# Performance work log

Hardware: AMD Instinct MI355X
Metric: run time of the kernel (lower is better)

Reference implementation:

```python
import jax, jax.numpy as jnp
import numpy as np

B, T, E, H = 8, 4096, 1024, 128

def setup_inputs() -> dict:
    key = jax.random.key(0)
    kx, kq, kk, kv = jax.random.split(key, 4)
    x = jax.random.normal(kx, (B, T, E), dtype=jnp.float32)
    # bias-free Linear weights stored as (in, out) for x @ W
    scale = 1.0 / np.sqrt(E)
    Wq = jax.random.normal(kq, (E, H), dtype=jnp.float32) * scale
    Wk = jax.random.normal(kk, (E, H), dtype=jnp.float32) * scale
    Wv = jax.random.normal(kv, (E, H), dtype=jnp.float32) * scale
    return {"x": x, "Wq": Wq, "Wk": Wk, "Wv": Wv}

def reference(x, Wq, Wk, Wv):
    # x: (B,T,E) -> out: (B,T,H). Causal single-head attention, dropout p=0 (no-op).
    q = x @ Wq  # (B,T,H)
    k = x @ Wk
    v = x @ Wv
    head_norm = jnp.sqrt(jnp.float32(q.shape[-1]))
    att = jnp.einsum('bth,bsh->bts', q, k) / head_norm  # (B,T,T)
    causal = jnp.tril(jnp.ones((x.shape[1], x.shape[1]), dtype=bool))
    att = jnp.where(causal, att, -jnp.inf)
    att = jax.nn.softmax(att, axis=-1)
    return jnp.einsum('bts,bsh->bth', att, v)
```

## Files before the change

kernel.cpp:

```cpp
#include <hip/hip_runtime.h>
#include <hip/hip_bf16.h>
#include <stdint.h>

#define Bn 8
#define Tn 4096
#define En 1024
#define Hn 128
#define SCALE 0.08838834764831845f

typedef __attribute__((ext_vector_type(8))) short bf16x8;
typedef __attribute__((ext_vector_type(4))) float f32x4;

__device__ __forceinline__ float bf2f(unsigned short v) {
    return __uint_as_float(((unsigned int)v) << 16);
}
__device__ __forceinline__ unsigned int pkbf(float a, float b) {
    __hip_bfloat162 h = __float22bfloat162_rn(make_float2(a, b));
    union { __hip_bfloat162 h2; unsigned int u; } cv;
    cv.h2 = h;
    return cv.u;
}

__device__ __forceinline__ void gll16(const unsigned short* g, unsigned short* l) {
    __builtin_amdgcn_global_load_lds(
        (const __attribute__((address_space(1))) void*)g,
        (__attribute__((address_space(3))) void*)l, 16, 0, 0);
}

__global__ __launch_bounds__(256)
void xcvt(const float* __restrict__ x, unsigned short* __restrict__ xb) {
    const size_t i = ((size_t)blockIdx.x * 256 + threadIdx.x) * 16;
    const float4* src = (const float4*)(x + i);
    float4 a = src[0], b = src[1], c = src[2], d = src[3];
    uint4 o0, o1;
    o0.x = pkbf(a.x, a.y); o0.y = pkbf(a.z, a.w);
    o0.z = pkbf(b.x, b.y); o0.w = pkbf(b.z, b.w);
    o1.x = pkbf(c.x, c.y); o1.y = pkbf(c.z, c.w);
    o1.z = pkbf(d.x, d.y); o1.w = pkbf(d.z, d.w);
    *(uint4*)(xb + i) = o0;
    *(uint4*)(xb + i + 8) = o1;
}

__global__ __launch_bounds__(256)
void wcvt(const float* __restrict__ Wq, const float* __restrict__ Wk,
          const float* __restrict__ Wv, unsigned short* __restrict__ wt3) {
    const int which = blockIdx.x;
    const int k0 = blockIdx.y * 128;
    const float* W = (which == 0) ? Wq : (which == 1) ? Wk : Wv;
    unsigned short* wt = wt3 + (size_t)which * 131072;

    __shared__ unsigned short wl[128 * 132];
    const int t = threadIdx.x;
#pragma unroll
    for (int i = 0; i < 16; ++i) {
        const int idx = t + i * 256;
        const int k = idx >> 5, c4 = idx & 31;
        float4 v = *(const float4*)&W[(size_t)(k0 + k) * Hn + c4 * 4];
        uint2 p;
        p.x = pkbf(v.x, v.y);
        p.y = pkbf(v.z, v.w);
        *(uint2*)&wl[k * 132 + c4 * 4] = p;
    }
    __syncthreads();
#pragma unroll
    for (int j = 0; j < 32; ++j) {
        const int idx = t + j * 256;
        const int n = idx >> 6, kp = idx & 63;
        unsigned int u = (unsigned int)wl[(2 * kp) * 132 + n] |
                         ((unsigned int)wl[(2 * kp + 1) * 132 + n] << 16);
        *(unsigned int*)&wt[(size_t)n * 1024 + k0 + 2 * kp] = u;
    }
}

#define QSWZ(r, c) (((r) << 7) + ((c) ^ (((r) & 7) << 4)))

__global__ __launch_bounds__(256)
void qkv2(const unsigned short* __restrict__ xb,
          const unsigned short* __restrict__ wt3,
          unsigned short* __restrict__ Qo,
          unsigned short* __restrict__ Ko,
          unsigned short* __restrict__ Vo) {
    const int mt = blockIdx.x;
    const int which = blockIdx.y;
    const unsigned short* wt = wt3 + (size_t)which * 131072;
    unsigned short* out = (which == 0) ? Qo : (which == 1) ? Ko : Vo;
    const float scale = (which == 0) ? SCALE : 1.0f;

    __shared__ alignas(16) unsigned short Xs[2][128 * 64];
    __shared__ alignas(16) unsigned short Ws[2][128 * 64];

    const int t = threadIdx.x;
    const int w = t >> 6;
    const int lane = t & 63;
    const int quad = lane >> 4;
    const int l16 = lane & 15;
    const int r8 = lane >> 3;
    const int cb = lane & 7;

    const unsigned short* xtile = xb + (size_t)(mt * 128) * En;

    f32x4 acc[2][8];
#pragma unroll
    for (int mi = 0; mi < 2; ++mi)
#pragma unroll
        for (int nst = 0; nst < 8; ++nst) acc[mi][nst] = (f32x4){0.f, 0.f, 0.f, 0.f};

    auto stage = [&](int buf, int kt) {
#pragma unroll
        for (int i = 0; i < 4; ++i) {
            const int row = i * 32 + w * 8 + r8;
            gll16(xtile + (size_t)row * En + kt * 64 + ((cb ^ (row & 7)) * 8),
                  &Xs[buf][(i * 32 + w * 8) * 64]);
        }
#pragma unroll
        for (int i = 0; i < 4; ++i) {
            const int row = i * 32 + w * 8 + r8;
            gll16(wt + (size_t)row * 1024 + kt * 64 + ((cb ^ (row & 7)) * 8),
                  &Ws[buf][(i * 32 + w * 8) * 64]);
        }
    };

    stage(0, 0);
    __syncthreads();

    for (int kt = 0; kt < 16; ++kt) {
        const int buf = kt & 1;
        if (kt < 15) stage(buf ^ 1, kt + 1);
        const char* xs = (const char*)Xs[buf];
        const char* ws = (const char*)Ws[buf];
#pragma unroll
        for (int ks = 0; ks < 2; ++ks) {
            bf16x8 af[2];
#pragma unroll
            for (int mi = 0; mi < 2; ++mi)
                af[mi] = *(const bf16x8*)(xs + QSWZ(w * 32 + mi * 16 + l16, ks * 64 + quad * 16));
#pragma unroll
            for (int nst = 0; nst < 8; ++nst) {
                bf16x8 bfr = *(const bf16x8*)(ws + QSWZ(nst * 16 + l16, ks * 64 + quad * 16));
                acc[0][nst] = __builtin_amdgcn_mfma_f32_16x16x32_bf16(bfr, af[0], acc[0][nst], 0, 0, 0);
                acc[1][nst] = __builtin_amdgcn_mfma_f32_16x16x32_bf16(bfr, af[1], acc[1][nst], 0, 0, 0);
            }
        }
        if (kt < 15) __syncthreads();
    }

#pragma unroll
    for (int mi = 0; mi < 2; ++mi) {
        const size_t rowbase = (size_t)(mt * 128 + w * 32 + mi * 16 + l16) * Hn;
#pragma unroll
        for (int nst = 0; nst < 8; ++nst) {
            f32x4 v = acc[mi][nst];
            uint2 pk;
            pk.x = pkbf(v[0] * scale, v[1] * scale);
            pk.y = pkbf(v[2] * scale, v[3] * scale);
            *(uint2*)(out + rowbase + nst * 16 + quad * 4) = pk;
        }
    }
}

__global__ __launch_bounds__(256)
void qkv_mfma(const float* __restrict__ x,
              const float* __restrict__ Wq,
              const float* __restrict__ Wk,
              const float* __restrict__ Wv,
              unsigned short* __restrict__ Qo,
              unsigned short* __restrict__ Ko,
              unsigned short* __restrict__ Vo) {
    const int mt = blockIdx.x;
    const int which = blockIdx.y;
    const float* W = (which == 0) ? Wq : (which == 1) ? Wk : Wv;
    unsigned short* out = (which == 0) ? Qo : (which == 1) ? Ko : Vo;
    const float scale = (which == 0) ? SCALE : 1.0f;

    __shared__ alignas(16) unsigned short Xs[128 * 72];
    __shared__ alignas(16) unsigned short Wt[128 * 72];

    const int t = threadIdx.x;
    const int w = t >> 6;
    const int lane = t & 63;
    const int quad = lane >> 4;
    const int l16 = lane & 15;

    const int xrow = t >> 1;
    const int xkc = (t & 1) * 32;
    const int ws0 = (t & 31) * 2;
    const int wd0 = (t >> 5) * 16;

    const float* xsrc0 = x + (size_t)(mt * 128 + xrow) * En + xkc;

    f32x4 acc[2][8];
#pragma unroll
    for (int mi = 0; mi < 2; ++mi)
#pragma unroll
        for (int nst = 0; nst < 8; ++nst) acc[mi][nst] = (f32x4){0.f, 0.f, 0.f, 0.f};

    float4 xpre[8], wpre[8];
    {
        const float* src = xsrc0;
#pragma unroll
        for (int i = 0; i < 8; ++i) xpre[i] = *(const float4*)(src + i * 4);
        const float* w0 = W + (size_t)ws0 * Hn + wd0;
        const float* w1 = w0 + Hn;
#pragma unroll
        for (int i = 0; i < 4; ++i) wpre[i] = *(const float4*)(w0 + i * 4);
#pragma unroll
        for (int i = 0; i < 4; ++i) wpre[4 + i] = *(const float4*)(w1 + i * 4);
    }

    for (int kt = 0; kt < 16; ++kt) {
        __syncthreads();
        {
            unsigned int u[16];
#pragma unroll
            for (int i = 0; i < 8; ++i) {
                u[2 * i]     = pkbf(xpre[i].x, xpre[i].y);
                u[2 * i + 1] = pkbf(xpre[i].z, xpre[i].w);
            }
#pragma unroll
            for (int i = 0; i < 4; ++i)
                *(uint4*)&Xs[xrow * 72 + xkc + i * 8] = ((const uint4*)u)[i];

            const float* ax = (const float*)&wpre[0];
            const float* bx = (const float*)&wpre[4];
#pragma unroll
            for (int dd = 0; dd < 16; ++dd)
                *(unsigned int*)&Wt[(wd0 + dd) * 72 + ws0] = pkbf(ax[dd], bx[dd]);
        }
        if (kt < 15) {
            const float* src = xsrc0 + (kt + 1) * 64;
#pragma unroll
            for (int i = 0; i < 8; ++i) xpre[i] = *(const float4*)(src + i * 4);
            const float* w0 = W + (size_t)((kt + 1) * 64 + ws0) * Hn + wd0;
            const float* w1 = w0 + Hn;
#pragma unroll
            for (int i = 0; i < 4; ++i) wpre[i] = *(const float4*)(w0 + i * 4);
#pragma unroll
            for (int i = 0; i < 4; ++i) wpre[4 + i] = *(const float4*)(w1 + i * 4);
        }
        __syncthreads();

#pragma unroll
        for (int ks = 0; ks < 2; ++ks) {
            bf16x8 af[2];
#pragma unroll
            for (int mi = 0; mi < 2; ++mi)
                af[mi] = *(const bf16x8*)&Xs[(w * 32 + mi * 16 + l16) * 72 + ks * 32 + quad * 8];
#pragma unroll
            for (int nst = 0; nst < 8; ++nst) {
                bf16x8 bfr = *(const bf16x8*)&Wt[(nst * 16 + l16) * 72 + ks * 32 + quad * 8];
                acc[0][nst] = __builtin_amdgcn_mfma_f32_16x16x32_bf16(bfr, af[0], acc[0][nst], 0, 0, 0);
                acc[1][nst] = __builtin_amdgcn_mfma_f32_16x16x32_bf16(bfr, af[1], acc[1][nst], 0, 0, 0);
            }
        }
    }

#pragma unroll
    for (int mi = 0; mi < 2; ++mi) {
        const size_t rowbase = (size_t)(mt * 128 + w * 32 + mi * 16 + l16) * Hn;
#pragma unroll
        for (int nst = 0; nst < 8; ++nst) {
            f32x4 v = acc[mi][nst];
            uint2 pk;
            pk.x = pkbf(v[0] * scale, v[1] * scale);
            pk.y = pkbf(v[2] * scale, v[3] * scale);
            *(uint2*)(out + rowbase + nst * 16 + quad * 4) = pk;
        }
    }
}

#define KSWZ(r, c) (((r) << 8) + ((c) ^ (((r) & 7) << 4)))
#define VSWZ(r, c) (((r) << 7) + ((c) ^ (((r) & 7) << 4)))

__global__ __launch_bounds__(512, 4)
void flash_mfma(const unsigned short* __restrict__ Qb,
                const unsigned short* __restrict__ Kb,
                const unsigned short* __restrict__ Vb,
                float* __restrict__ out) {
    const int b = blockIdx.x;
    const int bx = blockIdx.y;
    const int qt = (bx < 32) ? (63 - bx) : (bx - 32);
    const int t = threadIdx.x;
    const int w = t >> 6;
    const int g = w >> 2;
    const int rg = w & 3;
    const int lane = t & 63;
    const int quad = lane >> 4;
    const int l16 = lane & 15;
    const int t256 = t & 255;

    extern __shared__ unsigned short pool[];
    char* const poolb = (char*)pool;
    char* const Kg = poolb + g * 16384;
    char* const Vg = poolb + 32768 + g * 16384;
    char* const Pw = poolb + 65536 + w * 2048;
    float* const Os = (float*)poolb;
    float* const Ex = (float*)(poolb + 40960);
    float* const Em = (float*)(poolb + 73728);
    float* const El = Em + 64;

    const size_t gbase = (size_t)b * ((size_t)Tn * Hn);
    const unsigned short* kbase = Kb + gbase;
    const unsigned short* vbase = Vb + gbase;

    const int l_hi = lane >> 4;
    const int cpr = (lane & 15) * 16;
    const int vs0 = (t256 & 31) * 2;
    const int vd0 = (t256 >> 5) * 16;

    uint4 vra, vrb, vrc, vrd;
    if (g <= qt) {
        const unsigned short* vsrc = vbase + (size_t)(g * 64) * Hn;
        vra = *(const uint4*)&vsrc[vs0 * 128 + vd0];
        vrb = *(const uint4*)&vsrc[vs0 * 128 + vd0 + 8];
        vrc = *(const uint4*)&vsrc[(vs0 + 1) * 128 + vd0];
        vrd = *(const uint4*)&vsrc[(vs0 + 1) * 128 + vd0 + 8];
    }

    {
        const unsigned short* qsrc = Qb + gbase + (size_t)(qt * 64) * Hn;
#pragma unroll
        for (int i = 0; i < 2; ++i) {
            const int row = w * 8 + i * 4 + l_hi;
            const int scol = cpr ^ ((row & 7) << 4);
            gll16(qsrc + row * 128 + (scol >> 1),
                  (unsigned short*)(poolb + w * 2048 + i * 1024));
        }
    }
    __syncthreads();

    bf16x8 qf[4];
#pragma unroll
    for (int ks = 0; ks < 4; ++ks)
        qf[ks] = *(const bf16x8*)(poolb + KSWZ(rg * 16 + l16, ks * 64 + quad * 16));

    f32x4 acc_o[8];
#pragma unroll
    for (int i = 0; i < 8; ++i) acc_o[i] = (f32x4){0.f, 0.f, 0.f, 0.f};
    float m_run = -1e30f, l_run = 0.f;

    const int n = (qt >> 1) + 1;
    for (int it = 0; it < n; ++it) {
        const int kt = 2 * it + g;
        const bool active = (kt <= qt);
        __syncthreads();
        if (active) {
            const unsigned short* ktile = kbase + (size_t)(kt * 64) * Hn;
#pragma unroll
            for (int i = 0; i < 4; ++i) {
                const int row = rg * 16 + i * 4 + l_hi;
                const int scol = cpr ^ ((row & 7) << 4);
                gll16(ktile + row * 128 + (scol >> 1),
                      (unsigned short*)(Kg + rg * 4096 + i * 1024));
            }
            const unsigned short* pa = (const unsigned short*)&vra;
            const unsigned short* pb = (const unsigned short*)&vrb;
            const unsigned short* pc = (const unsigned short*)&vrc;
            const unsigned short* pd = (const unsigned short*)&vrd;
#pragma unroll
            for (int dd = 0; dd < 8; ++dd)
                *(unsigned int*)(Vg + VSWZ(vd0 + dd, vs0 * 2)) =
                    (unsigned int)pa[dd] | ((unsigned int)pc[dd] << 16);
#pragma unroll
            for (int dd = 0; dd < 8; ++dd)
                *(unsigned int*)(Vg + VSWZ(vd0 + 8 + dd, vs0 * 2)) =
                    (unsigned int)pb[dd] | ((unsigned int)pd[dd] << 16);
        }
        __syncthreads();
        if (kt + 2 <= qt) {
            const unsigned short* vsrc = vbase + (size_t)((kt + 2) * 64) * Hn;
            vra = *(const uint4*)&vsrc[vs0 * 128 + vd0];
            vrb = *(const uint4*)&vsrc[vs0 * 128 + vd0 + 8];
            vrc = *(const uint4*)&vsrc[(vs0 + 1) * 128 + vd0];
            vrd = *(const uint4*)&vsrc[(vs0 + 1) * 128 + vd0 + 8];
        }
        if (!active) continue;

        const bool diag = (kt == qt);
        f32x4 sa[4];
#pragma unroll
        for (int st = 0; st < 4; ++st) {
            if (diag && st > rg) {
                sa[st] = (f32x4){-1e30f, -1e30f, -1e30f, -1e30f};
            } else {
                f32x4 c = (f32x4){0.f, 0.f, 0.f, 0.f};
#pragma unroll
                for (int ks = 0; ks < 4; ++ks) {
                    bf16x8 kf = *(const bf16x8*)(Kg + KSWZ(st * 16 + l16, ks * 64 + quad * 16));
                    c = __builtin_amdgcn_mfma_f32_16x16x32_bf16(kf, qf[ks], c, 0, 0, 0);
                }
                if (diag && st == rg) {
#pragma unroll
                    for (int r = 0; r < 4; ++r)
                        if (quad * 4 + r > l16) c[r] = -1e30f;
                }
                sa[st] = c;
            }
        }

        float mloc = -1e30f;
#pragma unroll
        for (int st = 0; st < 4; ++st)
#pragma unroll
            for (int r = 0; r < 4; ++r) mloc = fmaxf(mloc, sa[st][r]);
        mloc = fmaxf(mloc, __shfl_xor(mloc, 16));
        mloc = fmaxf(mloc, __shfl_xor(mloc, 32));
        const float m_new = fmaxf(m_run, mloc);
        const float alpha = __expf(m_run - m_new);
        float lsum = 0.f;
#pragma unroll
        for (int st = 0; st < 4; ++st)
#pragma unroll
            for (int r = 0; r < 4; ++r) {
                const float e = __expf(sa[st][r] - m_new);
                sa[st][r] = e;
                lsum += e;
            }
        lsum += __shfl_xor(lsum, 16);
        lsum += __shfl_xor(lsum, 32);
        l_run = l_run * alpha + lsum;
        m_run = m_new;
#pragma unroll
        for (int i = 0; i < 8; ++i) acc_o[i] *= alpha;

#pragma unroll
        for (int st = 0; st < 4; ++st) {
            uint2 pk;
            pk.x = pkbf(sa[st][0], sa[st][1]);
            pk.y = pkbf(sa[st][2], sa[st][3]);
            *(uint2*)(Pw + VSWZ(l16, st * 32 + quad * 8)) = pk;
        }
        bf16x8 pf0 = *(const bf16x8*)(Pw + VSWZ(l16, quad * 16));
        bf16x8 pf1 = *(const bf16x8*)(Pw + VSWZ(l16, 64 + quad * 16));

#pragma unroll
        for (int dt = 0; dt < 8; ++dt) {
            bf16x8 vf0 = *(const bf16x8*)(Vg + VSWZ(dt * 16 + l16, quad * 16));
            acc_o[dt] = __builtin_amdgcn_mfma_f32_16x16x32_bf16(vf0, pf0, acc_o[dt], 0, 0, 0);
            bf16x8 vf1 = *(const bf16x8*)(Vg + VSWZ(dt * 16 + l16, 64 + quad * 16));
            acc_o[dt] = __builtin_amdgcn_mfma_f32_16x16x32_bf16(vf1, pf1, acc_o[dt], 0, 0, 0);
        }
    }

    __syncthreads();
    if (g == 1) {
        float* dst = Ex + (rg * 16 + l16) * 128;
#pragma unroll
        for (int dt = 0; dt < 8; ++dt)
            *(f32x4*)&dst[dt * 16 + quad * 4] = acc_o[dt];
        if (quad == 0) {
            Em[rg * 16 + l16] = m_run;
            El[rg * 16 + l16] = l_run;
        }
    }
    __syncthreads();
    if (g == 0) {
        const float* src = Ex + (rg * 16 + l16) * 128;
        const float m2 = Em[rg * 16 + l16];
        const float l2 = El[rg * 16 + l16];
        const float ms = fmaxf(m_run, m2);
        const float a1 = __expf(m_run - ms);
        const float a2 = __expf(m2 - ms);
        const float linv = 1.f / (l_run * a1 + l2 * a2);
#pragma unroll
        for (int dt = 0; dt < 8; ++dt) {
            f32x4 o2 = *(const f32x4*)&src[dt * 16 + quad * 4];
            f32x4 v = (acc_o[dt] * a1 + o2 * a2) * linv;
            *(f32x4*)&Os[(rg * 16 + l16) * 132 + dt * 16 + quad * 4] = v;
        }
    }
    __syncthreads();
    float* dst = out + gbase + (size_t)(qt * 64) * Hn;
#pragma unroll
    for (int i = 0; i < 4; ++i) {
        const int idx = (t + i * 512) * 4;
        const int row = idx >> 7, col = idx & 127;
        *(float4*)&dst[row * 128 + col] = *(const float4*)&Os[row * 132 + col];
    }
}

extern "C" void kernel_launch(void* const* d_in, const int* in_sizes, int n_in,
                              void* d_out, int out_size, void* d_ws, size_t ws_size,
                              hipStream_t stream) {
    const float* x  = (const float*)d_in[0];
    const float* Wq = (const float*)d_in[1];
    const float* Wk = (const float*)d_in[2];
    const float* Wv = (const float*)d_in[3];
    float* o = (float*)d_out;

    const size_t qkvb = (size_t)Bn * Tn * Hn;
    unsigned short* Qb = (unsigned short*)d_ws;
    unsigned short* Kb = Qb + qkvb;
    unsigned short* Vb = Kb + qkvb;
    unsigned short* xbf = Vb + qkvb;
    unsigned short* wt3 = xbf + (size_t)Bn * Tn * En;

    const size_t ws_need = (3 * qkvb + (size_t)Bn * Tn * En + 3 * (size_t)Hn * En)
                           * sizeof(unsigned short);

    static bool attr_done = false;
    if (!attr_done) {
        hipFuncSetAttribute((const void*)flash_mfma,
                            hipFuncAttributeMaxDynamicSharedMemorySize, 81920);
        attr_done = true;
    }

    if (ws_size >= ws_need) {
        xcvt<<<8192, 256, 0, stream>>>(x, xbf);
        wcvt<<<dim3(3, 8), 256, 0, stream>>>(Wq, Wk, Wv, wt3);
        qkv2<<<dim3(256, 3), 256, 0, stream>>>(xbf, wt3, Qb, Kb, Vb);
    } else {
        qkv_mfma<<<dim3(256, 3), 256, 0, stream>>>(x, Wq, Wk, Wv, Qb, Kb, Vb);
    }
    flash_mfma<<<dim3(8, 64), 512, 81920, stream>>>(Qb, Kb, Vb, o);
}
```

Measured before the change: 356.5 us.

## Halve flash block to 4 waves, each computing two 16-row query strips

The attention kernel now launches 256 threads (4 waves) per block instead of 512. Each wave handles 32 query rows as two 16-row sub-tiles and reuses every K fragment loaded from LDS across both sub-tiles, and every V fragment across both P operands. This cuts LDS reads per MFMA and barrier participants, but doubles the accumulator and Q-fragment registers per wave, which lowers occupancy. Each thread also stages twice as much of the K/V tile, and the number of blocks is unchanged.

```diff
diff --git a/kernel.cpp b/kernel.cpp
--- a/kernel.cpp
+++ b/kernel.cpp
@@ -271,7 +271,7 @@
 #define KSWZ(r, c) (((r) << 8) + ((c) ^ (((r) & 7) << 4)))
 #define VSWZ(r, c) (((r) << 7) + ((c) ^ (((r) & 7) << 4)))
 
-__global__ __launch_bounds__(512, 4)
+__global__ __launch_bounds__(256, 2)
 void flash_mfma(const unsigned short* __restrict__ Qb,
                 const unsigned short* __restrict__ Kb,
                 const unsigned short* __restrict__ Vb,
@@ -281,18 +281,18 @@
     const int qt = (bx < 32) ? (63 - bx) : (bx - 32);
     const int t = threadIdx.x;
     const int w = t >> 6;
-    const int g = w >> 2;
-    const int rg = w & 3;
+    const int g = w >> 1;
+    const int rg = w & 1;
     const int lane = t & 63;
     const int quad = lane >> 4;
     const int l16 = lane & 15;
-    const int t256 = t & 255;
+    const int t128 = t & 127;
 
     extern __shared__ unsigned short pool[];
     char* const poolb = (char*)pool;
     char* const Kg = poolb + g * 16384;
     char* const Vg = poolb + 32768 + g * 16384;
-    char* const Pw = poolb + 65536 + w * 2048;
+    char* const Pw = poolb + 65536 + w * 4096;
     float* const Os = (float*)poolb;
     float* const Ex = (float*)(poolb + 40960);
     float* const Em = (float*)(poolb + 73728);
@@ -304,39 +304,48 @@
 
     const int l_hi = lane >> 4;
     const int cpr = (lane & 15) * 16;
-    const int vs0 = (t256 & 31) * 2;
-    const int vd0 = (t256 >> 5) * 16;
-
-    uint4 vra, vrb, vrc, vrd;
+    const int vs0 = (t128 & 31) * 2;
+    const int vd0 = (t128 >> 5) * 32;
+
+    uint4 va0, va1, va2, va3, vb0, vb1, vb2, vb3;
     if (g <= qt) {
         const unsigned short* vsrc = vbase + (size_t)(g * 64) * Hn;
-        vra = *(const uint4*)&vsrc[vs0 * 128 + vd0];
-        vrb = *(const uint4*)&vsrc[vs0 * 128 + vd0 + 8];
-        vrc = *(const uint4*)&vsrc[(vs0 + 1) * 128 + vd0];
-        vrd = *(const uint4*)&vsrc[(vs0 + 1) * 128 + vd0 + 8];
+        va0 = *(const uint4*)&vsrc[vs0 * 128 + vd0];
+        va1 = *(const uint4*)&vsrc[vs0 * 128 + vd0 + 8];
+        va2 = *(const uint4*)&vsrc[vs0 * 128 + vd0 + 16];
+        va3 = *(const uint4*)&vsrc[vs0 * 128 + vd0 + 24];
+        vb0 = *(const uint4*)&vsrc[(vs0 + 1) * 128 + vd0];
+        vb1 = *(const uint4*)&vsrc[(vs0 + 1) * 128 + vd0 + 8];
+        vb2 = *(const uint4*)&vsrc[(vs0 + 1) * 128 + vd0 + 16];
+        vb3 = *(const uint4*)&vsrc[(vs0 + 1) * 128 + vd0 + 24];
     }
 
     {
         const unsigned short* qsrc = Qb + gbase + (size_t)(qt * 64) * Hn;
 #pragma unroll
-        for (int i = 0; i < 2; ++i) {
-            const int row = w * 8 + i * 4 + l_hi;
+        for (int i = 0; i < 4; ++i) {
+            const int row = w * 16 + i * 4 + l_hi;
             const int scol = cpr ^ ((row & 7) << 4);
             gll16(qsrc + row * 128 + (scol >> 1),
-                  (unsigned short*)(poolb + w * 2048 + i * 1024));
+                  (unsigned short*)(poolb + w * 4096 + i * 1024));
         }
     }
     __syncthreads();
 
-    bf16x8 qf[4];
-#pragma unroll
-    for (int ks = 0; ks < 4; ++ks)
-        qf[ks] = *(const bf16x8*)(poolb + KSWZ(rg * 16 + l16, ks * 64 + quad * 16));
-
-    f32x4 acc_o[8];
-#pragma unroll
-    for (int i = 0; i < 8; ++i) acc_o[i] = (f32x4){0.f, 0.f, 0.f, 0.f};
-    float m_run = -1e30f, l_run = 0.f;
+    bf16x8 qf[2][4];
+#pragma unroll
+    for (int s = 0; s < 2; ++s)
+#pragma unroll
+        for (int ks = 0; ks < 4; ++ks)
+            qf[s][ks] = *(const bf16x8*)(poolb + KSWZ(rg * 32 + s * 16 + l16, ks * 64 + quad * 16));
+
+    f32x4 acc_o[2][8];
+#pragma unroll
+    for (int s = 0; s < 2; ++s)
+#pragma unroll
+        for (int i = 0; i < 8; ++i) acc_o[s][i] = (f32x4){0.f, 0.f, 0.f, 0.f};
+    float m_run[2] = {-1e30f, -1e30f};
+    float l_run[2] = {0.f, 0.f};
 
     const int n = (qt >> 1) + 1;
     for (int it = 0; it < n; ++it) {
@@ -346,133 +355,175 @@
         if (active) {
             const unsigned short* ktile = kbase + (size_t)(kt * 64) * Hn;
 #pragma unroll
-            for (int i = 0; i < 4; ++i) {
-                const int row = rg * 16 + i * 4 + l_hi;
+            for (int i = 0; i < 8; ++i) {
+                const int row = rg * 32 + i * 4 + l_hi;
                 const int scol = cpr ^ ((row & 7) << 4);
                 gll16(ktile + row * 128 + (scol >> 1),
-                      (unsigned short*)(Kg + rg * 4096 + i * 1024));
-            }
-            const unsigned short* pa = (const unsigned short*)&vra;
-            const unsigned short* pb = (const unsigned short*)&vrb;
-            const unsigned short* pc = (const unsigned short*)&vrc;
-            const unsigned short* pd = (const unsigned short*)&vrd;
+                      (unsigned short*)(Kg + rg * 8192 + i * 1024));
+            }
+            const unsigned short* pa0 = (const unsigned short*)&va0;
+            const unsigned short* pa1 = (const unsigned short*)&va1;
+            const unsigned short* pa2 = (const unsigned short*)&va2;
+            const unsigned short* pa3 = (const unsigned short*)&va3;
+            const unsigned short* pb0 = (const unsigned short*)&vb0;
+            const unsigned short* pb1 = (const unsigned short*)&vb1;
+            const unsigned short* pb2 = (const unsigned short*)&vb2;
+            const unsigned short* pb3 = (const unsigned short*)&vb3;
 #pragma unroll
             for (int dd = 0; dd < 8; ++dd)
                 *(unsigned int*)(Vg + VSWZ(vd0 + dd, vs0 * 2)) =
-                    (unsigned int)pa[dd] | ((unsigned int)pc[dd] << 16);
+                    (unsigned int)pa0[dd] | ((unsigned int)pb0[dd] << 16);
 #pragma unroll
             for (int dd = 0; dd < 8; ++dd)
                 *(unsigned int*)(Vg + VSWZ(vd0 + 8 + dd, vs0 * 2)) =
-                    (unsigned int)pb[dd] | ((unsigned int)pd[dd] << 16);
+                    (unsigned int)pa1[dd] | ((unsigned int)pb1[dd] << 16);
+#pragma unroll
+            for (int dd = 0; dd < 8; ++dd)
+                *(unsigned int*)(Vg + VSWZ(vd0 + 16 + dd, vs0 * 2)) =
+                    (unsigned int)pa2[dd] | ((unsigned int)pb2[dd] << 16);
+#pragma unroll
+            for (int dd = 0; dd < 8; ++dd)
+                *(unsigned int*)(Vg + VSWZ(vd0 + 24 + dd, vs0 * 2)) =
+                    (unsigned int)pa3[dd] | ((unsigned int)pb3[dd] << 16);
         }
         __syncthreads();
         if (kt + 2 <= qt) {
             const unsigned short* vsrc = vbase + (size_t)((kt + 2) * 64) * Hn;
-            vra = *(const uint4*)&vsrc[vs0 * 128 + vd0];
-            vrb = *(const uint4*)&vsrc[vs0 * 128 + vd0 + 8];
-            vrc = *(const uint4*)&vsrc[(vs0 + 1) * 128 + vd0];
-            vrd = *(const uint4*)&vsrc[(vs0 + 1) * 128 + vd0 + 8];
+            va0 = *(const uint4*)&vsrc[vs0 * 128 + vd0];
+            va1 = *(const uint4*)&vsrc[vs0 * 128 + vd0 + 8];
+            va2 = *(const uint4*)&vsrc[vs0 * 128 + vd0 + 16];
+            va3 = *(const uint4*)&vsrc[vs0 * 128 + vd0 + 24];
+            vb0 = *(const uint4*)&vsrc[(vs0 + 1) * 128 + vd0];
+            vb1 = *(const uint4*)&vsrc[(vs0 + 1) * 128 + vd0 + 8];
+            vb2 = *(const uint4*)&vsrc[(vs0 + 1) * 128 + vd0 + 16];
+            vb3 = *(const uint4*)&vsrc[(vs0 + 1) * 128 + vd0 + 24];
         }
         if (!active) continue;
 
         const bool diag = (kt == qt);
-        f32x4 sa[4];
+        f32x4 sa[2][4];
 #pragma unroll
         for (int st = 0; st < 4; ++st) {
-            if (diag && st > rg) {
-                sa[st] = (f32x4){-1e30f, -1e30f, -1e30f, -1e30f};
-            } else {
-                f32x4 c = (f32x4){0.f, 0.f, 0.f, 0.f};
-#pragma unroll
-                for (int ks = 0; ks < 4; ++ks) {
-                    bf16x8 kf = *(const bf16x8*)(Kg + KSWZ(st * 16 + l16, ks * 64 + quad * 16));
-                    c = __builtin_amdgcn_mfma_f32_16x16x32_bf16(kf, qf[ks], c, 0, 0, 0);
+            const bool skipAll = diag && (st > rg * 2 + 1);
+            bf16x8 kf[4];
+            if (!skipAll) {
+#pragma unroll
+                for (int ks = 0; ks < 4; ++ks)
+                    kf[ks] = *(const bf16x8*)(Kg + KSWZ(st * 16 + l16, ks * 64 + quad * 16));
+            }
+#pragma unroll
+            for (int s = 0; s < 2; ++s) {
+                const int qs = rg * 2 + s;
+                if (diag && st > qs) {
+                    sa[s][st] = (f32x4){-1e30f, -1e30f, -1e30f, -1e30f};
+                } else {
+                    f32x4 c = (f32x4){0.f, 0.f, 0.f, 0.f};
+#pragma unroll
+                    for (int ks = 0; ks < 4; ++ks)
+                        c = __builtin_amdgcn_mfma_f32_16x16x32_bf16(kf[ks], qf[s][ks], c, 0, 0, 0);
+                    if (diag && st == qs) {
+#pragma unroll
+                        for (int r = 0; r < 4; ++r)
+                            if (quad * 4 + r > l16) c[r] = -1e30f;
+                    }
+                    sa[s][st] = c;
                 }
-                if (diag && st == rg) {
-#pragma unroll
-                    for (int r = 0; r < 4; ++r)
-                        if (quad * 4 + r > l16) c[r] = -1e30f;
+            }
+        }
+
+#pragma unroll
+        for (int s = 0; s < 2; ++s) {
+            float mloc = -1e30f;
+#pragma unroll
+            for (int st = 0; st < 4; ++st)
+#pragma unroll
+                for (int r = 0; r < 4; ++r) mloc = fmaxf(mloc, sa[s][st][r]);
+            mloc = fmaxf(mloc, __shfl_xor(mloc, 16));
+            mloc = fmaxf(mloc, __shfl_xor(mloc, 32));
+            const float m_new = fmaxf(m_run[s], mloc);
+            const float alpha = __expf(m_run[s] - m_new);
+            float lsum = 0.f;
+#pragma unroll
+            for (int st = 0; st < 4; ++st)
+#pragma unroll
+                for (int r = 0; r < 4; ++r) {
+                    const float e = __expf(sa[s][st][r] - m_new);
+                    sa[s][st][r] = e;
+                    lsum += e;
                 }
-                sa[st] = c;
-            }
-        }
-
-        float mloc = -1e30f;
-#pragma unroll
-        for (int st = 0; st < 4; ++st)
-#pragma unroll
-            for (int r = 0; r < 4; ++r) mloc = fmaxf(mloc, sa[st][r]);
-        mloc = fmaxf(mloc, __shfl_xor(mloc, 16));
-        mloc = fmaxf(mloc, __shfl_xor(mloc, 32));
-        const float m_new = fmaxf(m_run, mloc);
-        const float alpha = __expf(m_run - m_new);
-        float lsum = 0.f;
-#pragma unroll
-        for (int st = 0; st < 4; ++st)
-#pragma unroll
-            for (int r = 0; r < 4; ++r) {
-                const float e = __expf(sa[st][r] - m_new);
-                sa[st][r] = e;
-                lsum += e;
-            }
-        lsum += __shfl_xor(lsum, 16);
-        lsum += __shfl_xor(lsum, 32);
-        l_run = l_run * alpha + lsum;
-        m_run = m_new;
-#pragma unroll
-        for (int i = 0; i < 8; ++i) acc_o[i] *= alpha;
-
-#pragma unroll
-        for (int st = 0; st < 4; ++st) {
-            uint2 pk;
-            pk.x = pkbf(sa[st][0], sa[st][1]);
-            pk.y = pkbf(sa[st][2], sa[st][3]);
-            *(uint2*)(Pw + VSWZ(l16, st * 32 + quad * 8)) = pk;
-        }
-        bf16x8 pf0 = *(const bf16x8*)(Pw + VSWZ(l16, quad * 16));
-        bf16x8 pf1 = *(const bf16x8*)(Pw + VSWZ(l16, 64 + quad * 16));
+            lsum += __shfl_xor(lsum, 16);
+            lsum += __shfl_xor(lsum, 32);
+            l_run[s] = l_run[s] * alpha + lsum;
+            m_run[s] = m_new;
+#pragma unroll
+            for (int i = 0; i < 8; ++i) acc_o[s][i] *= alpha;
+#pragma unroll
+            for (int st = 0; st < 4; ++st) {
+                uint2 pk;
+                pk.x = pkbf(sa[s][st][0], sa[s][st][1]);
+                pk.y = pkbf(sa[s][st][2], sa[s][st][3]);
+                *(uint2*)(Pw + VSWZ(s * 16 + l16, st * 32 + quad * 8)) = pk;
+            }
+        }
+        bf16x8 pf[2][2];
+#pragma unroll
+        for (int s = 0; s < 2; ++s) {
+            pf[s][0] = *(const bf16x8*)(Pw + VSWZ(s * 16 + l16, quad * 16));
+            pf[s][1] = *(const bf16x8*)(Pw + VSWZ(s * 16 + l16, 64 + quad * 16));
+        }
 
 #pragma unroll
         for (int dt = 0; dt < 8; ++dt) {
             bf16x8 vf0 = *(const bf16x8*)(Vg + VSWZ(dt * 16 + l16, quad * 16));
-            acc_o[dt] = __builtin_amdgcn_mfma_f32_16x16x32_bf16(vf0, pf0, acc_o[dt], 0, 0, 0);
             bf16x8 vf1 = *(const bf16x8*)(Vg + VSWZ(dt * 16 + l16, 64 + quad * 16));
-            acc_o[dt] = __builtin_amdgcn_mfma_f32_16x16x32_bf16(vf1, pf1, acc_o[dt], 0, 0, 0);
+#pragma unroll
+            for (int s = 0; s < 2; ++s) {
+                acc_o[s][dt] = __builtin_amdgcn_mfma_f32_16x16x32_bf16(vf0, pf[s][0], acc_o[s][dt], 0, 0, 0);
+                acc_o[s][dt] = __builtin_amdgcn_mfma_f32_16x16x32_bf16(vf1, pf[s][1], acc_o[s][dt], 0, 0, 0);
+            }
         }
     }
 
     __syncthreads();
     if (g == 1) {
-        float* dst = Ex + (rg * 16 + l16) * 128;
-#pragma unroll
-        for (int dt = 0; dt < 8; ++dt)
-            *(f32x4*)&dst[dt * 16 + quad * 4] = acc_o[dt];
-        if (quad == 0) {
-            Em[rg * 16 + l16] = m_run;
-            El[rg * 16 + l16] = l_run;
+#pragma unroll
+        for (int s = 0; s < 2; ++s) {
+            const int row = rg * 32 + s * 16 + l16;
+            float* dst = Ex + row * 128;
+#pragma unroll
+            for (int dt = 0; dt < 8; ++dt)
+                *(f32x4*)&dst[dt * 16 + quad * 4] = acc_o[s][dt];
+            if (quad == 0) {
+                Em[row] = m_run[s];
+                El[row] = l_run[s];
+            }
         }
     }
     __syncthreads();
     if (g == 0) {
-        const float* src = Ex + (rg * 16 + l16) * 128;
-        const float m2 = Em[rg * 16 + l16];
-        const float l2 = El[rg * 16 + l16];
-        const float ms = fmaxf(m_run, m2);
-        const float a1 = __expf(m_run - ms);
-        const float a2 = __expf(m2 - ms);
-        const float linv = 1.f / (l_run * a1 + l2 * a2);
-#pragma unroll
-        for (int dt = 0; dt < 8; ++dt) {
-            f32x4 o2 = *(const f32x4*)&src[dt * 16 + quad * 4];
-            f32x4 v = (acc_o[dt] * a1 + o2 * a2) * linv;
-            *(f32x4*)&Os[(rg * 16 + l16) * 132 + dt * 16 + quad * 4] = v;
+#pragma unroll
+        for (int s = 0; s < 2; ++s) {
+            const int row = rg * 32 + s * 16 + l16;
+            const float* src = Ex + row * 128;
+            const float m2 = Em[row];
+            const float l2 = El[row];
+            const float ms = fmaxf(m_run[s], m2);
+            const float a1 = __expf(m_run[s] - ms);
+            const float a2 = __expf(m2 - ms);
+            const float linv = 1.f / (l_run[s] * a1 + l2 * a2);
+#pragma unroll
+            for (int dt = 0; dt < 8; ++dt) {
+                f32x4 o2 = *(const f32x4*)&src[dt * 16 + quad * 4];
+                f32x4 v = (acc_o[s][dt] * a1 + o2 * a2) * linv;
+                *(f32x4*)&Os[row * 132 + dt * 16 + quad * 4] = v;
+            }
         }
     }
     __syncthreads();
     float* dst = out + gbase + (size_t)(qt * 64) * Hn;
 #pragma unroll
-    for (int i = 0; i < 4; ++i) {
-        const int idx = (t + i * 512) * 4;
+    for (int i = 0; i < 8; ++i) {
+        const int idx = (t + i * 256) * 4;
         const int row = idx >> 7, col = idx & 127;
         *(float4*)&dst[row * 128 + col] = *(const float4*)&Os[row * 132 + col];
     }
@@ -511,5 +562,5 @@
     } else {
         qkv_mfma<<<dim3(256, 3), 256, 0, stream>>>(x, Wq, Wk, Wv, Qb, Kb, Vb);
     }
-    flash_mfma<<<dim3(8, 64), 512, 81920, stream>>>(Qb, Kb, Vb, o);
-}
+    flash_mfma<<<dim3(8, 64), 256, 81920, stream>>>(Qb, Kb, Vb, o);
+}
```

After: 357.4 us. No clear change (+0.3%).

## Use 512-thread QKV blocks and lazy softmax rescaling in flash kernel

Applied to the files above, without the earlier changes.

The QKV projection kernel now runs 8 waves per block, each owning 16 rows instead of 32, which halves accumulator registers per thread and raises occupancy. Staging is redistributed so each wave loads 16 rows of X and W. In the flash attention loop the running max and output rescale are skipped unless a new tile max exceeds the old one by more than a threshold, and the max reduction becomes a tree. Lazy rescaling stays exact in the final normalization but lets exponentials grow up to e^8, a small precision risk in bf16 P values.

```diff
diff --git a/kernel.cpp b/kernel.cpp
--- a/kernel.cpp
+++ b/kernel.cpp
@@ -74,7 +74,7 @@
 
 #define QSWZ(r, c) (((r) << 7) + ((c) ^ (((r) & 7) << 4)))
 
-__global__ __launch_bounds__(256)
+__global__ __launch_bounds__(512, 4)
 void qkv2(const unsigned short* __restrict__ xb,
           const unsigned short* __restrict__ wt3,
           unsigned short* __restrict__ Qo,
@@ -99,24 +99,22 @@
 
     const unsigned short* xtile = xb + (size_t)(mt * 128) * En;
 
-    f32x4 acc[2][8];
-#pragma unroll
-    for (int mi = 0; mi < 2; ++mi)
-#pragma unroll
-        for (int nst = 0; nst < 8; ++nst) acc[mi][nst] = (f32x4){0.f, 0.f, 0.f, 0.f};
+    f32x4 acc[8];
+#pragma unroll
+    for (int nst = 0; nst < 8; ++nst) acc[nst] = (f32x4){0.f, 0.f, 0.f, 0.f};
 
     auto stage = [&](int buf, int kt) {
 #pragma unroll
-        for (int i = 0; i < 4; ++i) {
-            const int row = i * 32 + w * 8 + r8;
+        for (int i = 0; i < 2; ++i) {
+            const int row = w * 16 + i * 8 + r8;
             gll16(xtile + (size_t)row * En + kt * 64 + ((cb ^ (row & 7)) * 8),
-                  &Xs[buf][(i * 32 + w * 8) * 64]);
-        }
-#pragma unroll
-        for (int i = 0; i < 4; ++i) {
-            const int row = i * 32 + w * 8 + r8;
+                  &Xs[buf][(w * 16 + i * 8) * 64]);
+        }
+#pragma unroll
+        for (int i = 0; i < 2; ++i) {
+            const int row = w * 16 + i * 8 + r8;
             gll16(wt + (size_t)row * 1024 + kt * 64 + ((cb ^ (row & 7)) * 8),
-                  &Ws[buf][(i * 32 + w * 8) * 64]);
+                  &Ws[buf][(w * 16 + i * 8) * 64]);
         }
     };
 
@@ -130,26 +128,21 @@
         const char* ws = (const char*)Ws[buf];
 #pragma unroll
         for (int ks = 0; ks < 2; ++ks) {
-            bf16x8 af[2];
-#pragma unroll
-            for (int mi = 0; mi < 2; ++mi)
-                af[mi] = *(const bf16x8*)(xs + QSWZ(w * 32 + mi * 16 + l16, ks * 64 + quad * 16));
+            bf16x8 af = *(const bf16x8*)(xs + QSWZ(w * 16 + l16, ks * 64 + quad * 16));
 #pragma unroll
             for (int nst = 0; nst < 8; ++nst) {
                 bf16x8 bfr = *(const bf16x8*)(ws + QSWZ(nst * 16 + l16, ks * 64 + quad * 16));
-                acc[0][nst] = __builtin_amdgcn_mfma_f32_16x16x32_bf16(bfr, af[0], acc[0][nst], 0, 0, 0);
-                acc[1][nst] = __builtin_amdgcn_mfma_f32_16x16x32_bf16(bfr, af[1], acc[1][nst], 0, 0, 0);
+                acc[nst] = __builtin_amdgcn_mfma_f32_16x16x32_bf16(bfr, af, acc[nst], 0, 0, 0);
             }
         }
         if (kt < 15) __syncthreads();
     }
 
-#pragma unroll
-    for (int mi = 0; mi < 2; ++mi) {
-        const size_t rowbase = (size_t)(mt * 128 + w * 32 + mi * 16 + l16) * Hn;
+    {
+        const size_t rowbase = (size_t)(mt * 128 + w * 16 + l16) * Hn;
 #pragma unroll
         for (int nst = 0; nst < 8; ++nst) {
-            f32x4 v = acc[mi][nst];
+            f32x4 v = acc[nst];
             uint2 pk;
             pk.x = pkbf(v[0] * scale, v[1] * scale);
             pk.y = pkbf(v[2] * scale, v[3] * scale);
@@ -397,30 +390,34 @@
             }
         }
 
-        float mloc = -1e30f;
-#pragma unroll
-        for (int st = 0; st < 4; ++st)
-#pragma unroll
-            for (int r = 0; r < 4; ++r) mloc = fmaxf(mloc, sa[st][r]);
+        float t0 = fmaxf(fmaxf(sa[0][0], sa[0][1]), fmaxf(sa[0][2], sa[0][3]));
+        float t1 = fmaxf(fmaxf(sa[1][0], sa[1][1]), fmaxf(sa[1][2], sa[1][3]));
+        float t2 = fmaxf(fmaxf(sa[2][0], sa[2][1]), fmaxf(sa[2][2], sa[2][3]));
+        float t3 = fmaxf(fmaxf(sa[3][0], sa[3][1]), fmaxf(sa[3][2], sa[3][3]));
+        float mloc = fmaxf(fmaxf(t0, t1), fmaxf(t2, t3));
         mloc = fmaxf(mloc, __shfl_xor(mloc, 16));
         mloc = fmaxf(mloc, __shfl_xor(mloc, 32));
-        const float m_new = fmaxf(m_run, mloc);
-        const float alpha = __expf(m_run - m_new);
+
+        if (!__all(mloc <= m_run + 8.0f)) {
+            const float m_new = fmaxf(m_run, mloc);
+            const float alpha = __expf(m_run - m_new);
+            l_run *= alpha;
+#pragma unroll
+            for (int i = 0; i < 8; ++i) acc_o[i] *= alpha;
+            m_run = m_new;
+        }
         float lsum = 0.f;
 #pragma unroll
         for (int st = 0; st < 4; ++st)
 #pragma unroll
             for (int r = 0; r < 4; ++r) {
-                const float e = __expf(sa[st][r] - m_new);
+                const float e = __expf(sa[st][r] - m_run);
                 sa[st][r] = e;
                 lsum += e;
             }
         lsum += __shfl_xor(lsum, 16);
         lsum += __shfl_xor(lsum, 32);
-        l_run = l_run * alpha + lsum;
-        m_run = m_new;
-#pragma unroll
-        for (int i = 0; i < 8; ++i) acc_o[i] *= alpha;
+        l_run += lsum;
 
 #pragma unroll
         for (int st = 0; st < 4; ++st) {
@@ -507,7 +504,7 @@
     if (ws_size >= ws_need) {
         xcvt<<<8192, 256, 0, stream>>>(x, xbf);
         wcvt<<<dim3(3, 8), 256, 0, stream>>>(Wq, Wk, Wv, wt3);
-        qkv2<<<dim3(256, 3), 256, 0, stream>>>(xbf, wt3, Qb, Kb, Vb);
+        qkv2<<<dim3(256, 3), 512, 0, stream>>>(xbf, wt3, Qb, Kb, Vb);
     } else {
         qkv_mfma<<<dim3(256, 3), 256, 0, stream>>>(x, Wq, Wk, Wv, Qb, Kb, Vb);
     }
```

Result: faster. 346.9 us (-2.7%).
